# Performance work log

Hardware: AMD Instinct MI355X
Metric: run time of the kernel (lower is better)

The kernel has to match this reference:

```python
import jax, jax.numpy as jnp
import numpy as np

DIM = 768; NH = 8; G = 14; N = G * G + 1; B = 64; PD = DIM // 16; HID = 4 * DIM
SCOPES = (1, 4, 7)


def _build_adj(fs, scope):
    # windowed adjacency on an fs x fs grid, padded with an always-on ACM (class) token
    idx = np.arange(fs)
    ii, jj = np.meshgrid(idx, idx, indexing='ij')
    ri, rj = ii.ravel(), jj.ravel()
    a = ((np.abs(ri[:, None] - ri[None, :]) <= scope) & (np.abs(rj[:, None] - rj[None, :]) <= scope)).astype(np.float32)
    out = np.ones((fs * fs + 1, fs * fs + 1), np.float32)
    out[1:, 1:] = a
    return out


def _prior_adj():
    # loop=0 -> loop1=loop2=0, repeat = NH//4; heads get [adj1,adj1,adj2,adj2,adj3,adj3,ones,ones]
    rep = NH // 4
    mats = [_build_adj(G, s) for s in SCOPES] + [np.ones((N, N), np.float32)]
    return np.stack([m for m in mats for _ in range(rep)], 0)


def _rel_idx():
    coords = np.stack(np.meshgrid(np.arange(G), np.arange(G), indexing='ij')).reshape(2, -1)
    rel = (coords[:, :, None] - coords[:, None, :]).transpose(1, 2, 0).copy()
    rel[..., 0] += G - 1
    rel[..., 1] += G - 1
    rel[..., 0] *= 2 * G - 1
    idx = rel.sum(-1)
    out = np.full((N, N), (2 * G - 1) ** 2 + 1, np.int32)
    out[1:, 1:] = idx
    return out


def _biases():
    r = np.arange(-G, G + 1)  # arange(1-(G+1), G+1)
    g = np.stack(np.meshgrid(r, r, indexing='ij')).reshape(2, -1).T
    return g.astype(np.float32)  # ((2G+1)^2, 2)


def setup_inputs():
    key = jax.random.key(0)
    ks = iter(jax.random.split(key, 32))
    rn = lambda *s: jax.random.normal(next(ks), s, jnp.float32) * 0.02
    return dict(
        x=jax.random.normal(next(ks), (B, N, DIM), jnp.float32),
        norm1_w=jnp.ones(DIM), norm1_b=jnp.zeros(DIM),
        qkv_w=rn(3 * DIM, DIM),
        scale=10.0 * jnp.ones((NH, 1, 1)),
        pp_w=rn(PD, 2), pp_b=jnp.zeros(PD),
        ln1_w=jnp.ones(PD), ln1_b=jnp.zeros(PD), fcp1_w=rn(PD, PD), fcp1_b=jnp.zeros(PD),
        ln2_w=jnp.ones(PD), ln2_b=jnp.zeros(PD), fcp2_w=rn(PD, PD), fcp2_b=jnp.zeros(PD),
        ln3_w=jnp.ones(PD), ln3_b=jnp.zeros(PD), fcp3_w=rn(NH, PD), fcp3_b=jnp.zeros(NH),
        pre_w=rn(NH, NH) + jnp.eye(NH), post_w=rn(NH, NH) + jnp.eye(NH),
        proj_w=rn(DIM, DIM), proj_b=jnp.zeros(DIM),
        norm2_w=jnp.ones(DIM), norm2_b=jnp.zeros(DIM),
        m1_w=rn(HID, DIM), m1_b=jnp.zeros(HID),
        m2_w=rn(DIM, HID), m2_b=jnp.zeros(DIM),
        prior_adj=jnp.asarray(_prior_adj()),
        biases=jnp.asarray(_biases()),
        rel_idx=jnp.asarray(_rel_idx()),
    )


def _ln(x, w, b, eps=1e-5):
    m = x.mean(-1, keepdims=True)
    v = ((x - m) ** 2).mean(-1, keepdims=True)
    return (x - m) / jnp.sqrt(v + eps) * w + b


def _l2n(x, eps=1e-12):
    return x / jnp.maximum(jnp.linalg.norm(x, axis=-1, keepdims=True), eps)


def reference(x, norm1_w, norm1_b, qkv_w, scale, pp_w, pp_b, ln1_w, ln1_b, fcp1_w, fcp1_b, ln2_w, ln2_b, fcp2_w, fcp2_b, ln3_w, ln3_b, fcp3_w, fcp3_b, pre_w, post_w, proj_w, proj_b, norm2_w, norm2_b, m1_w, m1_b, m2_w, m2_b, prior_adj, biases, rel_idx):
    Bq, Nq, C = x.shape
    d = C // NH
    h = _ln(x, norm1_w, norm1_b)
    qkv = (h @ qkv_w.T).reshape(Bq, Nq, 3, NH, d).transpose(2, 0, 3, 1, 4)
    q, k, v = qkv[0], qkv[1], qkv[2]  # each (B, NH, N, d)
    attn = jnp.einsum('bhnd,bhmd->bhnm', _l2n(q), _l2n(k)) * jnp.minimum(scale, 100.0)[None]
    p = biases @ pp_w.T + pp_b
    p = jax.nn.relu(_ln(p, ln1_w, ln1_b)) @ fcp1_w.T + fcp1_b
    p = jax.nn.relu(_ln(p, ln2_w, ln2_b)) @ fcp2_w.T + fcp2_b
    p = jax.nn.relu(_ln(p, ln3_w, ln3_b)) @ fcp3_w.T + fcp3_b  # (841, NH)
    rpb = p[rel_idx]  # (N, N, NH)
    attn = attn + rpb.transpose(2, 0, 1)[None]
    attn = jnp.einsum('oh,bhnm->bonm', pre_w, attn)  # 1x1 conv over heads (pre-softmax)
    attn = jnp.where(prior_adj[None] > 0, attn, -1e9)
    attn = jax.nn.softmax(attn, axis=-1)
    attn = jnp.einsum('oh,bhnm->bonm', post_w, attn)  # 1x1 conv over heads (post-softmax)
    out = jnp.einsum('bhnm,bhmd->bhnd', attn, v).transpose(0, 2, 1, 3).reshape(Bq, Nq, C)
    x = x + (out @ proj_w.T + proj_b)
    h2 = _ln(x, norm2_w, norm2_b)
    h2 = jax.nn.gelu(h2 @ m1_w.T + m1_b, approximate=False) @ m2_w.T + m2_b
    return x + h2
```

## Files before the change

### kernel.cpp

```cpp
#include <hip/hip_runtime.h>
#include <hip/hip_bf16.h>
#include <math.h>

typedef __hip_bfloat16 bf16;
typedef __attribute__((ext_vector_type(8))) short bf16x8;
typedef __attribute__((ext_vector_type(4))) float f32x4;

__device__ __forceinline__ float b2f(bf16 x){ return __bfloat162float(x); }
__device__ __forceinline__ bf16  f2b(float x){ return __float2bfloat16(x); }
__device__ __forceinline__ float us2f(unsigned short u){ bf16 t; *(unsigned short*)&t = u; return __bfloat162float(t); }

__device__ __forceinline__ void gld16(const bf16* g, bf16* l){
    __builtin_amdgcn_global_load_lds(
        (const __attribute__((address_space(1))) unsigned int*)g,
        (__attribute__((address_space(3))) unsigned int*)l, 16, 0, 0);
}

#define NTOK 197
#define NBATCH 64
#define NHEAD 8
#define DHEAD 96
#define DIMC 768
#define NROWS (NBATCH * NTOK)
#define VTS 224
#define SMS 200
#define SBS 224
#define MHALF 6304

#define OFF_P   0ull
#define OFF_W   32768ull
#define SZ_QKVW 3538944ull
#define SZ_PRJW 1179648ull
#define SZ_M1W  4718592ull
#define SZ_M2W  4718592ull
#define OFF_H   14188544ull
#define SZ_H    19365888ull
#define OFF_Q   33554432ull
#define OFF_K   52920320ull
#define OFF_V   72286208ull

__global__ __launch_bounds__(256) void w_cvt_all(
    const float* __restrict__ s0, const float* __restrict__ s1,
    const float* __restrict__ s2, const float* __restrict__ s3, bf16* __restrict__ d)
{
    int i = blockIdx.x*256 + threadIdx.x;
    const float* s; int off;
    if (i < 442368){ s=s0; off=i; }
    else if (i < 589824){ s=s1; off=i-442368; }
    else if (i < 1179648){ s=s2; off=i-589824; }
    else { s=s3; off=i-1179648; }
    float4 v = ((const float4*)s)[off];
    bf16 t[4] = {f2b(v.x), f2b(v.y), f2b(v.z), f2b(v.w)};
    ((ushort4*)d)[i] = *(ushort4*)t;
}

__global__ __launch_bounds__(64) void pos_mlp(
    const float* __restrict__ biases, const float* __restrict__ pp_w, const float* __restrict__ pp_b,
    const float* __restrict__ ln1w, const float* __restrict__ ln1b,
    const float* __restrict__ f1w,  const float* __restrict__ f1b,
    const float* __restrict__ ln2w, const float* __restrict__ ln2b,
    const float* __restrict__ f2w,  const float* __restrict__ f2b,
    const float* __restrict__ ln3w, const float* __restrict__ ln3b,
    const float* __restrict__ f3w,  const float* __restrict__ f3b,
    const float* __restrict__ pre_w,
    float* __restrict__ pout)
{
    const int row = blockIdx.x, j = threadIdx.x;
    __shared__ float va[48], vb[48], pf[8];
    float b0 = biases[row*2], b1 = biases[row*2+1];
    if (j < 48) va[j] = b0*pp_w[j*2] + b1*pp_w[j*2+1] + pp_b[j];
    __syncthreads();
    {   float s=0.f, s2=0.f;
        for (int i=0;i<48;i++){ float t=va[i]; s+=t; s2+=t*t; }
        float mean=s*(1.f/48.f), var=s2*(1.f/48.f)-mean*mean, inv=rsqrtf(var+1e-5f);
        float r=0.f;
        if (j < 48){
            r = f1b[j];
            for (int i=0;i<48;i++){
                float t = fmaxf((va[i]-mean)*inv*ln1w[i] + ln1b[i], 0.f);
                r += t * f1w[j*48+i];
            }
        }
        __syncthreads();
        if (j < 48) vb[j] = r;
    }
    __syncthreads();
    {   float s=0.f, s2=0.f;
        for (int i=0;i<48;i++){ float t=vb[i]; s+=t; s2+=t*t; }
        float mean=s*(1.f/48.f), var=s2*(1.f/48.f)-mean*mean, inv=rsqrtf(var+1e-5f);
        float r=0.f;
        if (j < 48){
            r = f2b[j];
            for (int i=0;i<48;i++){
                float t = fmaxf((vb[i]-mean)*inv*ln2w[i] + ln2b[i], 0.f);
                r += t * f2w[j*48+i];
            }
        }
        __syncthreads();
        if (j < 48) va[j] = r;
    }
    __syncthreads();
    {   float s=0.f, s2=0.f;
        for (int i=0;i<48;i++){ float t=va[i]; s+=t; s2+=t*t; }
        float mean=s*(1.f/48.f), var=s2*(1.f/48.f)-mean*mean, inv=rsqrtf(var+1e-5f);
        if (j < 8){
            float r = f3b[j];
            for (int i=0;i<48;i++){
                float t = fmaxf((va[i]-mean)*inv*ln3w[i] + ln3b[i], 0.f);
                r += t * f3w[j*48+i];
            }
            pf[j] = r;
        }
    }
    __syncthreads();
    if (j < 8){
        float s = 0.f;
        #pragma unroll
        for (int hh=0; hh<8; hh++) s += pre_w[j*8+hh]*pf[hh];
        pout[row*8+j] = s;
    }
}

template<typename TIN>
__global__ __launch_bounds__(256) void ln768(
    const TIN* __restrict__ x, const float* __restrict__ w, const float* __restrict__ b,
    bf16* __restrict__ out)
{
    const int row = blockIdx.x, tid = threadIdx.x;
    const int wv = tid >> 6, ln = tid & 63;
    __shared__ float rs[4], rs2[4];
    const TIN* xr = x + (size_t)row * DIMC;
    float v[4] = {0.f,0.f,0.f,0.f};
    if (tid < 192){
        if constexpr (sizeof(TIN) == 4){
            float4 t4 = ((const float4*)xr)[tid];
            v[0]=t4.x; v[1]=t4.y; v[2]=t4.z; v[3]=t4.w;
        } else {
            ushort4 t4 = ((const ushort4*)xr)[tid];
            v[0]=us2f(t4.x); v[1]=us2f(t4.y); v[2]=us2f(t4.z); v[3]=us2f(t4.w);
        }
    }
    float s = v[0]+v[1]+v[2]+v[3];
    float s2 = v[0]*v[0]+v[1]*v[1]+v[2]*v[2]+v[3]*v[3];
    #pragma unroll
    for (int off=32; off; off>>=1){ s += __shfl_xor(s,off,64); s2 += __shfl_xor(s2,off,64); }
    if (ln == 0){ rs[wv]=s; rs2[wv]=s2; }
    __syncthreads();
    s = rs[0]+rs[1]+rs[2]+rs[3]; s2 = rs2[0]+rs2[1]+rs2[2]+rs2[3];
    float mean = s*(1.f/768.f), var = s2*(1.f/768.f) - mean*mean;
    float inv = rsqrtf(var + 1e-5f);
    if (tid < 192){
        float4 w4 = ((const float4*)w)[tid];
        float4 b4 = ((const float4*)b)[tid];
        bf16 o[4];
        o[0] = f2b((v[0]-mean)*inv*w4.x + b4.x);
        o[1] = f2b((v[1]-mean)*inv*w4.y + b4.y);
        o[2] = f2b((v[2]-mean)*inv*w4.z + b4.z);
        o[3] = f2b((v[3]-mean)*inv*w4.w + b4.w);
        ((ushort4*)(out + (size_t)row*DIMC))[tid] = *(ushort4*)o;
    }
}

__global__ __launch_bounds__(256) void l2norm_qk(bf16* __restrict__ q, bf16* __restrict__ k,
                                                 const float* __restrict__ scale)
{
    const int wv = threadIdx.x >> 6, ln = threadIdx.x & 63;
    const int g = ln >> 4, j = ln & 15;
    const size_t NR = (size_t)NBATCH*NHEAD*NTOK;
    size_t row = (size_t)blockIdx.x*16 + wv*4 + g;
    bool isq = row < NR;
    bf16* ptr = isq ? (q + row*DHEAD) : (k + (row-NR)*DHEAD);
    float xv[8];
    float ss = 0.f;
    if (j < 12){
        bf16x8 vv = *(const bf16x8*)(ptr + j*8);
        #pragma unroll
        for (int e=0;e<8;e++){ float f = us2f((unsigned short)vv[e]); xv[e]=f; ss += f*f; }
    }
    #pragma unroll
    for (int off=8; off; off>>=1) ss += __shfl_xor(ss, off, 64);
    float inv = 1.f / fmaxf(sqrtf(ss), 1e-12f);
    if (isq){
        int h = (int)((row / NTOK) & (NHEAD-1));
        inv *= fminf(scale[h], 100.f);
    }
    if (j < 12){
        bf16x8 ov;
        #pragma unroll
        for (int e=0;e<8;e++){ bf16 t = f2b(xv[e]*inv); ov[e] = *(short*)&t; }
        *(bf16x8*)(ptr + j*8) = ov;
    }
}

__global__ __launch_bounds__(256) void attn_mfma(
    const bf16* __restrict__ q, const bf16* __restrict__ k, const bf16* __restrict__ vt,
    const float* __restrict__ p,
    const float* __restrict__ pre_w, const float* __restrict__ post_w,
    bf16* __restrict__ ao)
{
    const int id = blockIdx.x;
    const int r8 = id & 7, t8 = id >> 3;
    const int bx = t8 % 25, b = r8 + 8*(t8/25);
    const int n0 = bx*8;
    const int tid = threadIdx.x, wv = tid>>6, ln = tid&63;
    const int fr = ln&15, fq = ln>>4;
    __shared__ float S[NHEAD*8*SMS];
    __shared__ float s_pre[64], s_post[64];
    bf16* Sb = (bf16*)S;
    if (tid < 64){ s_pre[tid]=pre_w[tid]; s_post[tid]=post_w[tid]; }

    #pragma unroll
    for (int hh=0; hh<2; hh++){
        const int h = wv + hh*4;
        int qr = n0 + fr; if (qr > 196) qr = 196;
        const bf16* qrow = q + ((size_t)(b*NHEAD+h)*NTOK + qr)*DHEAD + fq*8;
        bf16x8 a0 = *(const bf16x8*)(qrow);
        bf16x8 a1 = *(const bf16x8*)(qrow+32);
        bf16x8 a2 = *(const bf16x8*)(qrow+64);
        const bf16* kb0 = k + (size_t)(b*NHEAD+h)*NTOK*DHEAD + fq*8;
        auto krow = [&](int mt){ int nr = mt*16+fr; if (nr>196) nr=196; return kb0 + (size_t)nr*DHEAD; };
        const bf16* kp0 = krow(0);
        bf16x8 c00 = *(const bf16x8*)(kp0), c01 = *(const bf16x8*)(kp0+32), c02 = *(const bf16x8*)(kp0+64);
        const bf16* kp1 = krow(1);
        bf16x8 c10 = *(const bf16x8*)(kp1), c11 = *(const bf16x8*)(kp1+32), c12 = *(const bf16x8*)(kp1+64);
        #pragma unroll
        for (int mt=0; mt<13; mt++){
            bf16x8 p0, p1, p2;
            if (mt < 11){
                const bf16* kn = krow(mt+2);
                p0 = *(const bf16x8*)(kn); p1 = *(const bf16x8*)(kn+32); p2 = *(const bf16x8*)(kn+64);
            }
            f32x4 acc = {};
            acc = __builtin_amdgcn_mfma_f32_16x16x32_bf16(a0, c00, acc,0,0,0);
            acc = __builtin_amdgcn_mfma_f32_16x16x32_bf16(a1, c01, acc,0,0,0);
            acc = __builtin_amdgcn_mfma_f32_16x16x32_bf16(a2, c02, acc,0,0,0);
            int col = mt*16 + fr;
            if (fq < 2 && col < SMS){
                #pragma unroll
                for (int i=0;i<4;i++)
                    S[(h*8 + fq*4+i)*SMS + col] = acc[i];
            }
            c00=c10; c01=c11; c02=c12;
            if (mt < 11){ c10=p0; c11=p1; c12=p2; }
        }
    }
    __syncthreads();

    {
        const int sco[8] = {1,1,4,4,7,7,1000,1000};
        const int nq = tid >> 5, l32 = tid & 31;
        int n = n0 + nq; if (n > 196) n = 196;
        const bool nAlways = (n == 0);
        int ri=0, ci=0;
        if (!nAlways){ ri=(n-1)/14; ci=(n-1)-ri*14; }
        for (int m = l32; m < SMS; m += 32){
            if (m >= 197){
                #pragma unroll
                for (int o=0;o<8;o++) S[(o*8+nq)*SMS+m] = -1e9f;
                continue;
            }
            bool always = nAlways || (m==0);
            int rj=0, cj=0;
            if (m > 0){ rj=(m-1)/14; cj=(m-1)-rj*14; }
            int dr = ri-rj; if (dr<0) dr=-dr;
            int dc = ci-cj; if (dc<0) dc=-dc;
            int idx = always ? 730 : (ri-rj+13)*27 + (ci-cj+13);
            const float* pv = p + idx*8;
            float sh[8];
            #pragma unroll
            for (int h2=0;h2<8;h2++) sh[h2] = S[(h2*8+nq)*SMS+m];
            float ov[8];
            #pragma unroll
            for (int o=0;o<8;o++){
                float v = pv[o];
                #pragma unroll
                for (int h2=0;h2<8;h2++) v += s_pre[o*8+h2]*sh[h2];
                bool on = always || (dr<=sco[o] && dc<=sco[o]);
                ov[o] = on ? v : -1e9f;
            }
            #pragma unroll
            for (int o=0;o<8;o++) S[(o*8+nq)*SMS+m] = ov[o];
        }
    }
    __syncthreads();

    {
        const int g = ln >> 4, l16 = ln & 15;
        #pragma unroll
        for (int rr=0; rr<4; rr++){
            float* row = &S[(wv*16 + rr*4 + g)*SMS];
            float mx = -3e38f;
            for (int m=l16; m<SMS; m+=16) mx = fmaxf(mx, row[m]);
            #pragma unroll
            for (int off=8; off; off>>=1) mx = fmaxf(mx, __shfl_xor(mx,off,64));
            float sum = 0.f;
            for (int m=l16; m<SMS; m+=16){ float e=__expf(row[m]-mx); row[m]=e; sum+=e; }
            #pragma unroll
            for (int off=8; off; off>>=1) sum += __shfl_xor(sum,off,64);
            float inv = 1.f/sum;
            for (int m=l16; m<SMS; m+=16) row[m] *= inv;
        }
    }
    __syncthreads();

    {
        const int nq = tid >> 5, l32 = tid & 31;
        float ov[7][8];
        #pragma unroll
        for (int kk=0; kk<7; kk++){
            int m = l32 + 32*kk;
            if (m < 197){
                float ph[8];
                #pragma unroll
                for (int o=0;o<8;o++) ph[o] = S[(o*8+nq)*SMS+m];
                #pragma unroll
                for (int o2=0;o2<8;o2++){
                    float v=0.f;
                    #pragma unroll
                    for (int o=0;o<8;o++) v += s_post[o2*8+o]*ph[o];
                    ov[kk][o2]=v;
                }
            }
        }
        __syncthreads();
        #pragma unroll
        for (int kk=0; kk<7; kk++){
            int m = l32 + 32*kk;
            #pragma unroll
            for (int o=0;o<8;o++)
                Sb[(o*8+nq)*SBS + m] = (m < 197) ? f2b(ov[kk][o]) : f2b(0.f);
        }
    }
    __syncthreads();

    const int frA = fr & 7;
    #pragma unroll
    for (int hh=0; hh<2; hh++){
        const int h = wv + hh*4;
        const bf16* vbase = vt + (size_t)(b*NHEAD+h)*DHEAD*VTS;
        bf16x8 pa[7];
        #pragma unroll
        for (int ks=0; ks<7; ks++)
            pa[ks] = *(const bf16x8*)(Sb + (h*8+frA)*SBS + ks*32 + fq*8);
        bf16x8 bv[7], bn[7];
        #pragma unroll
        for (int ks=0; ks<7; ks++)
            bv[ks] = *(const bf16x8*)(vbase + (size_t)fr*VTS + ks*32 + fq*8);
        #pragma unroll
        for (int dt=0; dt<6; dt++){
            if (dt < 5){
                #pragma unroll
                for (int ks=0; ks<7; ks++)
                    bn[ks] = *(const bf16x8*)(vbase + (size_t)((dt+1)*16+fr)*VTS + ks*32 + fq*8);
            }
            f32x4 acc = {};
            #pragma unroll
            for (int ks=0; ks<7; ks++)
                acc = __builtin_amdgcn_mfma_f32_16x16x32_bf16(pa[ks], bv[ks], acc,0,0,0);
            #pragma unroll
            for (int i=0;i<4;i++){
                int nq = fq*4+i, n = n0+nq;
                if (nq < 8 && n < NTOK)
                    ao[((size_t)b*NTOK+n)*DIMC + h*DHEAD + dt*16+fr] = f2b(acc[i]);
            }
            #pragma unroll
            for (int ks=0; ks<7; ks++) bv[ks] = bn[ks];
        }
    }
}

enum { EPI_QKV=0, EPI_X1=1, EPI_GELU=2, EPI_OUT=3 };

template<int EPI>
__global__ __launch_bounds__(256) void gemm128(
    const bf16* __restrict__ A, int lda, int M,
    const bf16* __restrict__ B, int ldb,
    int K,
    const float* __restrict__ bias,
    const float* __restrict__ resid_f,
    const bf16* __restrict__ resid_b,
    float* __restrict__ dst_f,
    bf16* __restrict__ dst_b, int lddb,
    int row_off,
    bf16* __restrict__ qo, bf16* __restrict__ ko, bf16* __restrict__ vto)
{
    __shared__ bf16 As[2*128*32];
    __shared__ bf16 Bs[2*128*32];
    const int tid = threadIdx.x;
    const int wv = tid >> 6, ln = tid & 63;
    const int fr = ln & 15, fq = ln >> 4;
    const int wr = (wv & 1)*64, wc = (wv >> 1)*64;
    const int m0 = blockIdx.y*128, n0 = blockIdx.x*128;
    const int lnrow = ln >> 2, lncol = (ln & 3)*8;
    f32x4 acc[4][4] = {};
    for (int k0=0; k0<K; k0+=64){
        #pragma unroll
        for (int t=0;t<2;t++){
            #pragma unroll
            for (int c=0;c<2;c++){
                int rA = m0 + (c*4+wv)*16 + lnrow;
                if (rA >= M) rA = M-1;
                gld16(A + (size_t)rA*lda + k0 + t*32 + lncol, &As[t*4096 + (c*4+wv)*16*32]);
                int rB = n0 + (c*4+wv)*16 + lnrow;
                gld16(B + (size_t)rB*ldb + k0 + t*32 + lncol, &Bs[t*4096 + (c*4+wv)*16*32]);
            }
        }
        __syncthreads();
        #pragma unroll
        for (int t=0;t<2;t++){
            bf16x8 af[4], bfv[4];
            #pragma unroll
            for (int i=0;i<4;i++){
                af[i]  = *(const bf16x8*)&As[t*4096 + (wr + i*16 + fr)*32 + fq*8];
                bfv[i] = *(const bf16x8*)&Bs[t*4096 + (wc + i*16 + fr)*32 + fq*8];
            }
            #pragma unroll
            for (int mi=0;mi<4;mi++)
                #pragma unroll
                for (int ni=0;ni<4;ni++)
                    acc[mi][ni] = __builtin_amdgcn_mfma_f32_16x16x32_bf16(af[mi], bfv[ni], acc[mi][ni],0,0,0);
        }
        __syncthreads();
    }
    #pragma unroll
    for (int mi=0;mi<4;mi++){
        #pragma unroll
        for (int ni=0;ni<4;ni++){
            #pragma unroll
            for (int i=0;i<4;i++){
                int row = m0 + wr + mi*16 + fq*4 + i;
                int col = n0 + wc + ni*16 + fr;
                if (row >= M) continue;
                float val = acc[mi][ni][i];
                if constexpr (EPI == EPI_QKV){
                    int which = col/768, rem = col - which*768;
                    int hh = rem/96, di = rem - hh*96;
                    int bb = row/NTOK, nn = row - bb*NTOK;
                    if (which == 0)      qo[(((size_t)bb*NHEAD+hh)*NTOK+nn)*DHEAD + di] = f2b(val);
                    else if (which == 1) ko[(((size_t)bb*NHEAD+hh)*NTOK+nn)*DHEAD + di] = f2b(val);
                    else {
                        vto[(((size_t)bb*NHEAD+hh)*DHEAD+di)*VTS + nn] = f2b(val);
                        if (nn < VTS - NTOK)
                            vto[(((size_t)bb*NHEAD+hh)*DHEAD+di)*VTS + NTOK + nn] = f2b(0.f);
                    }
                } else if constexpr (EPI == EPI_X1){
                    dst_b[(size_t)row*DIMC + col] = f2b(val + bias[col] + resid_f[(size_t)row*DIMC + col]);
                } else if constexpr (EPI == EPI_GELU){
                    float t = val + bias[col];
                    t = 0.5f*t*(1.f + erff(t*0.70710678118654752f));
                    dst_b[(size_t)row*lddb + col] = f2b(t);
                } else {
                    size_t g = (size_t)(row + row_off)*DIMC + col;
                    dst_f[g] = val + bias[col] + b2f(resid_b[g]);
                }
            }
        }
    }
}

extern "C" void kernel_launch(void* const* d_in, const int* in_sizes, int n_in,
                              void* d_out, int out_size, void* d_ws, size_t ws_size,
                              hipStream_t stream)
{
    const float* x        = (const float*)d_in[0];
    const float* norm1_w  = (const float*)d_in[1];
    const float* norm1_b  = (const float*)d_in[2];
    const float* qkv_w    = (const float*)d_in[3];
    const float* scale    = (const float*)d_in[4];
    const float* pp_w     = (const float*)d_in[5];
    const float* pp_b     = (const float*)d_in[6];
    const float* ln1_w    = (const float*)d_in[7];
    const float* ln1_b    = (const float*)d_in[8];
    const float* fcp1_w   = (const float*)d_in[9];
    const float* fcp1_b   = (const float*)d_in[10];
    const float* ln2_w    = (const float*)d_in[11];
    const float* ln2_b    = (const float*)d_in[12];
    const float* fcp2_w   = (const float*)d_in[13];
    const float* fcp2_b   = (const float*)d_in[14];
    const float* ln3_w    = (const float*)d_in[15];
    const float* ln3_b    = (const float*)d_in[16];
    const float* fcp3_w   = (const float*)d_in[17];
    const float* fcp3_b   = (const float*)d_in[18];
    const float* pre_w    = (const float*)d_in[19];
    const float* post_w   = (const float*)d_in[20];
    const float* proj_w   = (const float*)d_in[21];
    const float* proj_b   = (const float*)d_in[22];
    const float* nrm2_w   = (const float*)d_in[23];
    const float* nrm2_b   = (const float*)d_in[24];
    const float* m1_w     = (const float*)d_in[25];
    const float* m1_b     = (const float*)d_in[26];
    const float* m2_w     = (const float*)d_in[27];
    const float* m2_b     = (const float*)d_in[28];
    const float* biases   = (const float*)d_in[30];
    float* out = (float*)d_out;

    char* ws = (char*)d_ws;
    float* p      = (float*)(ws + OFF_P);
    bf16*  qkvw_b = (bf16*)(ws + OFF_W);
    bf16*  prjw_b = (bf16*)(ws + OFF_W + SZ_QKVW);
    bf16*  m1w_b  = (bf16*)(ws + OFF_W + SZ_QKVW + SZ_PRJW);
    bf16*  m2w_b  = (bf16*)(ws + OFF_W + SZ_QKVW + SZ_PRJW + SZ_M1W);
    bf16*  h   = (bf16*)(ws + OFF_H);
    bf16*  qb  = (bf16*)(ws + OFF_Q);
    bf16*  kb  = (bf16*)(ws + OFF_K);
    bf16*  vt  = (bf16*)(ws + OFF_V);
    bf16*  ao  = (bf16*)(ws + OFF_H);
    bf16*  x1b = (bf16*)(ws + OFF_V);
    bf16*  h2  = (bf16*)(ws + OFF_K);
    bf16*  mid = (bf16*)(ws + OFF_H);

    w_cvt_all<<<6912, 256, 0, stream>>>(qkv_w, proj_w, m1_w, m2_w, qkvw_b);
    pos_mlp<<<841, 64, 0, stream>>>(biases, pp_w, pp_b, ln1_w, ln1_b, fcp1_w, fcp1_b,
                                    ln2_w, ln2_b, fcp2_w, fcp2_b, ln3_w, ln3_b, fcp3_w, fcp3_b,
                                    pre_w, p);
    ln768<float><<<NROWS, 256, 0, stream>>>(x, norm1_w, norm1_b, h);
    gemm128<EPI_QKV><<<dim3(18, 99), 256, 0, stream>>>(
        h, DIMC, NROWS, qkvw_b, DIMC, DIMC, nullptr, nullptr, nullptr, nullptr,
        nullptr, 0, 0, qb, kb, vt);
    l2norm_qk<<<(NBATCH*NHEAD*NTOK*2)/16, 256, 0, stream>>>(qb, kb, scale);
    attn_mfma<<<1600, 256, 0, stream>>>(qb, kb, vt, p, pre_w, post_w, ao);
    gemm128<EPI_X1><<<dim3(6, 99), 256, 0, stream>>>(
        ao, DIMC, NROWS, prjw_b, DIMC, DIMC, proj_b, x, nullptr, nullptr,
        x1b, 0, 0, nullptr, nullptr, nullptr);
    ln768<bf16><<<NROWS, 256, 0, stream>>>(x1b, nrm2_w, nrm2_b, h2);
    for (int c=0; c<2; c++){
        const int r0 = c*MHALF;
        gemm128<EPI_GELU><<<dim3(24, 50), 256, 0, stream>>>(
            h2 + (size_t)r0*DIMC, DIMC, MHALF, m1w_b, DIMC, DIMC, m1_b,
            nullptr, nullptr, nullptr, mid, 3072, 0, nullptr, nullptr, nullptr);
        gemm128<EPI_OUT><<<dim3(6, 50), 256, 0, stream>>>(
            mid, 3072, MHALF, m2w_b, 3072, 3072, m2_b,
            nullptr, x1b, out, nullptr, 0, r0, nullptr, nullptr, nullptr);
    }
    (void)in_sizes; (void)n_in; (void)out_size; (void)ws_size;
}
```

Baseline: 787.1 us.

## Double attention block to 512 threads and add XCD-aware GEMM block remapping

The attention kernel now launches 512 threads so each of 8 waves handles a single head for QK^T and PV, where before 4 waves each looped over two heads. The bias/mask and post-mix phases are restricted to the first 256 threads, and the softmax row split is halved per wave. Separately, the GEMMs switch to a 1D grid whose block index is remapped so that consecutive tiles land on the same XCD, aiming to improve L2 reuse. These are two unrelated changes that trade more waves per block and idle threads in some phases for more latency hiding and better cache locality.

```diff
diff --git a/kernel.cpp b/kernel.cpp
--- a/kernel.cpp
+++ b/kernel.cpp
@@ -192,7 +192,7 @@
     }
 }
 
-__global__ __launch_bounds__(256) void attn_mfma(
+__global__ __launch_bounds__(512) void attn_mfma(
     const bf16* __restrict__ q, const bf16* __restrict__ k, const bf16* __restrict__ vt,
     const float* __restrict__ p,
     const float* __restrict__ pre_w, const float* __restrict__ post_w,
@@ -209,9 +209,8 @@
     bf16* Sb = (bf16*)S;
     if (tid < 64){ s_pre[tid]=pre_w[tid]; s_post[tid]=post_w[tid]; }
 
-    #pragma unroll
-    for (int hh=0; hh<2; hh++){
-        const int h = wv + hh*4;
+    {
+        const int h = wv;
         int qr = n0 + fr; if (qr > 196) qr = 196;
         const bf16* qrow = q + ((size_t)(b*NHEAD+h)*NTOK + qr)*DHEAD + fq*8;
         bf16x8 a0 = *(const bf16x8*)(qrow);
@@ -246,7 +245,7 @@
     }
     __syncthreads();
 
-    {
+    if (tid < 256){
         const int sco[8] = {1,1,4,4,7,7,1000,1000};
         const int nq = tid >> 5, l32 = tid & 31;
         int n = n0 + nq; if (n > 196) n = 196;
@@ -287,8 +286,8 @@
     {
         const int g = ln >> 4, l16 = ln & 15;
         #pragma unroll
-        for (int rr=0; rr<4; rr++){
-            float* row = &S[(wv*16 + rr*4 + g)*SMS];
+        for (int rr=0; rr<2; rr++){
+            float* row = &S[(wv*8 + rr*4 + g)*SMS];
             float mx = -3e38f;
             for (int m=l16; m<SMS; m+=16) mx = fmaxf(mx, row[m]);
             #pragma unroll
@@ -304,39 +303,42 @@
     __syncthreads();
 
     {
-        const int nq = tid >> 5, l32 = tid & 31;
+        const int nq = (tid >> 5) & 7, l32 = tid & 31;
         float ov[7][8];
-        #pragma unroll
-        for (int kk=0; kk<7; kk++){
-            int m = l32 + 32*kk;
-            if (m < 197){
-                float ph[8];
+        if (tid < 256){
+            #pragma unroll
+            for (int kk=0; kk<7; kk++){
+                int m = l32 + 32*kk;
+                if (m < 197){
+                    float ph[8];
+                    #pragma unroll
+                    for (int o=0;o<8;o++) ph[o] = S[(o*8+nq)*SMS+m];
+                    #pragma unroll
+                    for (int o2=0;o2<8;o2++){
+                        float v=0.f;
+                        #pragma unroll
+                        for (int o=0;o<8;o++) v += s_post[o2*8+o]*ph[o];
+                        ov[kk][o2]=v;
+                    }
+                }
+            }
+        }
+        __syncthreads();
+        if (tid < 256){
+            #pragma unroll
+            for (int kk=0; kk<7; kk++){
+                int m = l32 + 32*kk;
                 #pragma unroll
-                for (int o=0;o<8;o++) ph[o] = S[(o*8+nq)*SMS+m];
-                #pragma unroll
-                for (int o2=0;o2<8;o2++){
-                    float v=0.f;
-                    #pragma unroll
-                    for (int o=0;o<8;o++) v += s_post[o2*8+o]*ph[o];
-                    ov[kk][o2]=v;
-                }
-            }
-        }
-        __syncthreads();
-        #pragma unroll
-        for (int kk=0; kk<7; kk++){
-            int m = l32 + 32*kk;
-            #pragma unroll
-            for (int o=0;o<8;o++)
-                Sb[(o*8+nq)*SBS + m] = (m < 197) ? f2b(ov[kk][o]) : f2b(0.f);
-        }
-    }
-    __syncthreads();
-
-    const int frA = fr & 7;
-    #pragma unroll
-    for (int hh=0; hh<2; hh++){
-        const int h = wv + hh*4;
+                for (int o=0;o<8;o++)
+                    Sb[(o*8+nq)*SBS + m] = (m < 197) ? f2b(ov[kk][o]) : f2b(0.f);
+            }
+        }
+    }
+    __syncthreads();
+
+    {
+        const int frA = fr & 7;
+        const int h = wv;
         const bf16* vbase = vt + (size_t)(b*NHEAD+h)*DHEAD*VTS;
         bf16x8 pa[7];
         #pragma unroll
@@ -359,8 +361,8 @@
                 acc = __builtin_amdgcn_mfma_f32_16x16x32_bf16(pa[ks], bv[ks], acc,0,0,0);
             #pragma unroll
             for (int i=0;i<4;i++){
-                int nq = fq*4+i, n = n0+nq;
-                if (nq < 8 && n < NTOK)
+                int nqq = fq*4+i, n = n0+nqq;
+                if (nqq < 8 && n < NTOK)
                     ao[((size_t)b*NTOK+n)*DIMC + h*DHEAD + dt*16+fr] = f2b(acc[i]);
             }
             #pragma unroll
@@ -382,7 +384,8 @@
     float* __restrict__ dst_f,
     bf16* __restrict__ dst_b, int lddb,
     int row_off,
-    bf16* __restrict__ qo, bf16* __restrict__ ko, bf16* __restrict__ vto)
+    bf16* __restrict__ qo, bf16* __restrict__ ko, bf16* __restrict__ vto,
+    int nbx)
 {
     __shared__ bf16 As[2*128*32];
     __shared__ bf16 Bs[2*128*32];
@@ -390,7 +393,12 @@
     const int wv = tid >> 6, ln = tid & 63;
     const int fr = ln & 15, fq = ln >> 4;
     const int wr = (wv & 1)*64, wc = (wv >> 1)*64;
-    const int m0 = blockIdx.y*128, n0 = blockIdx.x*128;
+    const int nwgs = (int)gridDim.x;
+    const int xcd = blockIdx.x & 7;
+    const int qq = nwgs >> 3, rr = nwgs & 7;
+    const int wg = (xcd < rr ? xcd*(qq+1) : rr*(qq+1) + (xcd-rr)*qq) + ((int)blockIdx.x >> 3);
+    const int byi = wg / nbx, bxi = wg - byi*nbx;
+    const int m0 = byi*128, n0 = bxi*128;
     const int lnrow = ln >> 2, lncol = (ln & 3)*8;
     f32x4 acc[4][4] = {};
     for (int k0=0; k0<K; k0+=64){
@@ -514,23 +522,23 @@
                                     ln2_w, ln2_b, fcp2_w, fcp2_b, ln3_w, ln3_b, fcp3_w, fcp3_b,
                                     pre_w, p);
     ln768<float><<<NROWS, 256, 0, stream>>>(x, norm1_w, norm1_b, h);
-    gemm128<EPI_QKV><<<dim3(18, 99), 256, 0, stream>>>(
+    gemm128<EPI_QKV><<<18*99, 256, 0, stream>>>(
         h, DIMC, NROWS, qkvw_b, DIMC, DIMC, nullptr, nullptr, nullptr, nullptr,
-        nullptr, 0, 0, qb, kb, vt);
+        nullptr, 0, 0, qb, kb, vt, 18);
     l2norm_qk<<<(NBATCH*NHEAD*NTOK*2)/16, 256, 0, stream>>>(qb, kb, scale);
-    attn_mfma<<<1600, 256, 0, stream>>>(qb, kb, vt, p, pre_w, post_w, ao);
-    gemm128<EPI_X1><<<dim3(6, 99), 256, 0, stream>>>(
+    attn_mfma<<<1600, 512, 0, stream>>>(qb, kb, vt, p, pre_w, post_w, ao);
+    gemm128<EPI_X1><<<6*99, 256, 0, stream>>>(
         ao, DIMC, NROWS, prjw_b, DIMC, DIMC, proj_b, x, nullptr, nullptr,
-        x1b, 0, 0, nullptr, nullptr, nullptr);
+        x1b, 0, 0, nullptr, nullptr, nullptr, 6);
     ln768<bf16><<<NROWS, 256, 0, stream>>>(x1b, nrm2_w, nrm2_b, h2);
     for (int c=0; c<2; c++){
         const int r0 = c*MHALF;
-        gemm128<EPI_GELU><<<dim3(24, 50), 256, 0, stream>>>(
+        gemm128<EPI_GELU><<<24*50, 256, 0, stream>>>(
             h2 + (size_t)r0*DIMC, DIMC, MHALF, m1w_b, DIMC, DIMC, m1_b,
-            nullptr, nullptr, nullptr, mid, 3072, 0, nullptr, nullptr, nullptr);
-        gemm128<EPI_OUT><<<dim3(6, 50), 256, 0, stream>>>(
+            nullptr, nullptr, nullptr, mid, 3072, 0, nullptr, nullptr, nullptr, 24);
+        gemm128<EPI_OUT><<<6*50, 256, 0, stream>>>(
             mid, 3072, MHALF, m2w_b, 3072, 3072, m2_b,
-            nullptr, x1b, out, nullptr, 0, r0, nullptr, nullptr, nullptr);
+            nullptr, x1b, out, nullptr, 0, r0, nullptr, nullptr, nullptr, 6);
     }
     (void)in_sizes; (void)n_in; (void)out_size; (void)ws_size;
 }
```

After: 780.7 us. About the same (-0.8%).
